# Kernel optimization log

Measured on AMD Instinct MI355X. Metric: run time of the kernel, lower is better.

Reference implementation:

```python
import jax, jax.numpy as jnp
import numpy as np

D_ATTN = 64


def setup_inputs() -> dict:
    key = jax.random.key(0)
    ks = jax.random.split(key, 10)
    B, N, D_MODEL = 8, 1024, 512
    s = 0.02
    return {
        "x": jax.random.normal(ks[0], (B, N, D_MODEL), jnp.float32),
        "top": jax.random.normal(ks[1], (B, N, N, 16), jnp.float32),
        "Wq": jax.random.normal(ks[2], (D_MODEL, D_ATTN), jnp.float32) * s,
        "bq": jnp.zeros((D_ATTN,), jnp.float32),
        "Wk": jax.random.normal(ks[3], (D_MODEL, D_ATTN), jnp.float32) * s,
        "bk": jnp.zeros((D_ATTN,), jnp.float32),
        "Wv": jax.random.normal(ks[4], (D_MODEL, D_ATTN), jnp.float32) * s,
        "bv": jnp.zeros((D_ATTN,), jnp.float32),
        "Wt": jax.random.normal(ks[5], (16, 1), jnp.float32) * s,
        "bt": jnp.zeros((1,), jnp.float32),
    }


def reference(x, top, Wq, bq, Wk, bk, Wv, bv, Wt, bt):
    # QKV projections: [B,N,d_model] -> [B,N,d_attn]
    Q = x @ Wq + bq
    K = x @ Wk + bk
    V = x @ Wv + bv
    scale = 1.0 / jnp.sqrt(jnp.asarray(D_ATTN, x.dtype))
    # [B,N,N] attention logits
    logits = jnp.einsum("bnd,bmd->bnm", Q, K) * scale
    # learned topological bias: Linear(16,1) on [B,N,N,16] -> [B,N,N]
    bias = jnp.einsum("bnmf,fo->bnmo", top, Wt)[..., 0] + bt[0]
    score = jax.nn.softmax(logits + bias, axis=-1)
    return jnp.einsum("bnm,bmd->bnd", score, V)
```

## Files before the change

kernel.cpp:

```cpp
#include <hip/hip_runtime.h>
#include <hip/hip_bf16.h>

typedef __attribute__((ext_vector_type(8))) short short8;
typedef __attribute__((ext_vector_type(4))) float f32x4;
typedef unsigned short ushort_t;
typedef unsigned int uint_t;

#define D_MODEL 512
#define D_ATTN  64

__device__ __forceinline__ ushort_t f2bf(float f) {
    uint_t u = __float_as_uint(f);
    u += 0x7FFFu + ((u >> 16) & 1u);
    return (ushort_t)(u >> 16);
}
__device__ __forceinline__ f32x4 ntload4(const f32x4* p) {
    return __builtin_nontemporal_load(p);
}

__global__ __launch_bounds__(256)
void qkv_all(const float* __restrict__ x,
             const float* __restrict__ Wq, const float* __restrict__ bq,
             const float* __restrict__ Wk, const float* __restrict__ bk,
             const float* __restrict__ Wv, const float* __restrict__ bv,
             ushort_t* __restrict__ Q, ushort_t* __restrict__ K,
             ushort_t* __restrict__ Vt)
{
    const int l = threadIdx.x & 63, w = threadIdx.x >> 6;
    const size_t bn0 = (size_t)blockIdx.x << 4;
    const int r0 = w << 2;
    const float* xb = x + (bn0 + r0) * D_MODEL;
    { uintptr_t u = (uintptr_t)xb; asm volatile("" : "+v"(u)); xb = (const float*)u; }

    float aq[4] = {0,0,0,0}, ak[4] = {0,0,0,0}, av[4] = {0,0,0,0};
#pragma unroll 2
    for (int k = 0; k < D_MODEL; k += 4) {
        float4 xr[4];
#pragma unroll
        for (int r = 0; r < 4; ++r) xr[r] = *(const float4*)(xb + r * D_MODEL + k);
        float wqv[4], wkv[4], wvv[4];
#pragma unroll
        for (int kk = 0; kk < 4; ++kk) {
            wqv[kk] = Wq[(k + kk) * D_ATTN + l];
            wkv[kk] = Wk[(k + kk) * D_ATTN + l];
            wvv[kk] = Wv[(k + kk) * D_ATTN + l];
        }
#pragma unroll
        for (int r = 0; r < 4; ++r) {
            const float xv[4] = {xr[r].x, xr[r].y, xr[r].z, xr[r].w};
#pragma unroll
            for (int kk = 0; kk < 4; ++kk) {
                aq[r] = fmaf(xv[kk], wqv[kk], aq[r]);
                ak[r] = fmaf(xv[kk], wkv[kk], ak[r]);
                av[r] = fmaf(xv[kk], wvv[kk], av[r]);
            }
        }
    }
    const float bqv = bq[l], bkv = bk[l], bvv = bv[l];
#pragma unroll
    for (int r = 0; r < 4; ++r) {
        Q[(bn0 + r0 + r) * D_ATTN + l] = f2bf((aq[r] + bqv) * 0.125f);
        K[(bn0 + r0 + r) * D_ATTN + l] = f2bf(ak[r] + bkv);
    }
    const int b = (int)(bn0 >> 10), n0loc = (int)(bn0 & 1023);
    uint2 pv;
    pv.x = (uint_t)f2bf(av[0] + bvv) | ((uint_t)f2bf(av[1] + bvv) << 16);
    pv.y = (uint_t)f2bf(av[2] + bvv) | ((uint_t)f2bf(av[3] + bvv) << 16);
    *(uint2*)(Vt + ((size_t)(b * 64 + l) << 10) + n0loc + r0) = pv;
}

__global__ __launch_bounds__(256)
void topo_attn_f(const float* __restrict__ top, const float* __restrict__ Wt,
                 const ushort_t* __restrict__ Q, const ushort_t* __restrict__ K,
                 const ushort_t* __restrict__ Vt, float* __restrict__ out)
{
    __shared__ float lds[16384];
    const int tid = threadIdx.x;
    const int l = tid & 63, wv = tid >> 6;
    const int b   = blockIdx.x >> 6;
    const int bn0 = blockIdx.x << 4;

    {
        const float* __restrict__ topb = top + ((size_t)bn0 << 14);
        const float4 wq = *(const float4*)(Wt + ((l & 3) << 2));
#pragma unroll
        for (int rr = 0; rr < 4; ++rr) {
            const int rloc = (wv << 2) + rr;
            const f32x4* gp = (const f32x4*)(topb + ((size_t)rloc << 14));
            float* ldsrow = lds + (rloc << 10);
#pragma unroll 2
            for (int g = 0; g < 16; ++g) {
                f32x4 v0 = ntload4(gp + (g << 8) + l);
                f32x4 v1 = ntload4(gp + (g << 8) + 64 + l);
                f32x4 v2 = ntload4(gp + (g << 8) + 128 + l);
                f32x4 v3 = ntload4(gp + (g << 8) + 192 + l);
                float p0 = v0[0] * wq.x; p0 = fmaf(v0[1], wq.y, p0); p0 = fmaf(v0[2], wq.z, p0); p0 = fmaf(v0[3], wq.w, p0);
                float p1 = v1[0] * wq.x; p1 = fmaf(v1[1], wq.y, p1); p1 = fmaf(v1[2], wq.z, p1); p1 = fmaf(v1[3], wq.w, p1);
                float p2 = v2[0] * wq.x; p2 = fmaf(v2[1], wq.y, p2); p2 = fmaf(v2[2], wq.z, p2); p2 = fmaf(v2[3], wq.w, p2);
                float p3 = v3[0] * wq.x; p3 = fmaf(v3[1], wq.y, p3); p3 = fmaf(v3[2], wq.z, p3); p3 = fmaf(v3[3], wq.w, p3);
                p0 += __shfl_xor(p0, 1); p0 += __shfl_xor(p0, 2);
                p1 += __shfl_xor(p1, 1); p1 += __shfl_xor(p1, 2);
                p2 += __shfl_xor(p2, 1); p2 += __shfl_xor(p2, 2);
                p3 += __shfl_xor(p3, 1); p3 += __shfl_xor(p3, 2);
                if (!(l & 3)) {
                    int mb = (g << 6) + (l >> 2);
                    ldsrow[mb]      = p0;
                    ldsrow[mb + 16] = p1;
                    ldsrow[mb + 32] = p2;
                    ldsrow[mb + 48] = p3;
                }
            }
        }
    }
    __syncthreads();

    const int lr = l & 15, lg = l >> 4;
    const short8 a0 = *(const short8*)(Q + ((size_t)(bn0 + lr)) * 64 + 8 * lg);
    const short8 a1 = *(const short8*)(Q + ((size_t)(bn0 + lr)) * 64 + 32 + 8 * lg);
    const ushort_t* __restrict__ Kb = K + ((size_t)b << 16);
#pragma unroll 4
    for (int t16 = 0; t16 < 16; ++t16) {
        int m0 = (wv << 8) + (t16 << 4);
        short8 kb0 = *(const short8*)(Kb + (size_t)(m0 + lr) * 64 + 8 * lg);
        short8 kb1 = *(const short8*)(Kb + (size_t)(m0 + lr) * 64 + 32 + 8 * lg);
        f32x4 acc = {0.f, 0.f, 0.f, 0.f};
        acc = __builtin_amdgcn_mfma_f32_16x16x32_bf16(a0, kb0, acc, 0, 0, 0);
        acc = __builtin_amdgcn_mfma_f32_16x16x32_bf16(a1, kb1, acc, 0, 0, 0);
#pragma unroll
        for (int j = 0; j < 4; ++j)
            lds[(4 * lg + j) * 1024 + m0 + lr] += acc[j];
    }
    __syncthreads();

    {
        const int r = tid >> 4, sseg = tid & 15;
        float4 v4[16];
        const float4* rowp = (const float4*)(lds + r * 1024 + sseg * 64);
#pragma unroll
        for (int i = 0; i < 16; ++i) v4[i] = rowp[i];
        __syncthreads();
        float mx = v4[0].x;
#pragma unroll
        for (int i = 0; i < 16; ++i)
            mx = fmaxf(mx, fmaxf(fmaxf(v4[i].x, v4[i].y), fmaxf(v4[i].z, v4[i].w)));
#pragma unroll
        for (int off = 8; off >= 1; off >>= 1) mx = fmaxf(mx, __shfl_xor(mx, off));
        float sum = 0.f;
#pragma unroll
        for (int i = 0; i < 16; ++i) {
            v4[i].x = __expf(v4[i].x - mx); sum += v4[i].x;
            v4[i].y = __expf(v4[i].y - mx); sum += v4[i].y;
            v4[i].z = __expf(v4[i].z - mx); sum += v4[i].z;
            v4[i].w = __expf(v4[i].w - mx); sum += v4[i].w;
        }
#pragma unroll
        for (int off = 8; off >= 1; off >>= 1) sum += __shfl_xor(sum, off);
        float inv = 1.0f / sum;
        ushort_t* pb = ((ushort_t*)lds) + r * 1024 + sseg * 64;
#pragma unroll
        for (int i = 0; i < 8; ++i) {
            uint_t w0 = (uint_t)f2bf(v4[2*i].x * inv)   | ((uint_t)f2bf(v4[2*i].y * inv)   << 16);
            uint_t w1 = (uint_t)f2bf(v4[2*i].z * inv)   | ((uint_t)f2bf(v4[2*i].w * inv)   << 16);
            uint_t w2 = (uint_t)f2bf(v4[2*i+1].x * inv) | ((uint_t)f2bf(v4[2*i+1].y * inv) << 16);
            uint_t w3 = (uint_t)f2bf(v4[2*i+1].z * inv) | ((uint_t)f2bf(v4[2*i+1].w * inv) << 16);
            ((uint4*)pb)[i] = make_uint4(w0, w1, w2, w3);
        }
    }
    __syncthreads();

    {
        f32x4 o[4] = {{0,0,0,0},{0,0,0,0},{0,0,0,0},{0,0,0,0}};
        const ushort_t* __restrict__ pb = ((const ushort_t*)lds) + lr * 1024;
        const ushort_t* __restrict__ Vb = Vt + ((size_t)b << 16);
#pragma unroll 2
        for (int c = 0; c < 8; ++c) {
            int m0 = (wv << 8) + (c << 5) + 8 * lg;
            short8 pa = *(const short8*)(pb + m0);
#pragma unroll
            for (int dt = 0; dt < 4; ++dt) {
                short8 vb = *(const short8*)(Vb + (size_t)(dt * 16 + lr) * 1024 + m0);
                o[dt] = __builtin_amdgcn_mfma_f32_16x16x32_bf16(pa, vb, o[dt], 0, 0, 0);
            }
        }
        float* lo = lds + 8192 + (wv << 10);
#pragma unroll
        for (int dt = 0; dt < 4; ++dt)
#pragma unroll
            for (int j = 0; j < 4; ++j)
                lo[(4 * lg + j) * 64 + dt * 16 + lr] = o[dt][j];
    }
    __syncthreads();

#pragma unroll
    for (int i = 0; i < 4; ++i) {
        int idx = (i << 8) + tid;
        float s2 = lds[8192 + idx] + lds[8192 + 1024 + idx]
                 + lds[8192 + 2048 + idx] + lds[8192 + 3072 + idx];
        out[((size_t)bn0 << 6) + idx] = s2;
    }
}

extern "C" void kernel_launch(void* const* d_in, const int* in_sizes, int n_in,
                              void* d_out, int out_size, void* d_ws, size_t ws_size,
                              hipStream_t stream) {
    const float* x   = (const float*)d_in[0];
    const float* top = (const float*)d_in[1];
    const float* Wq  = (const float*)d_in[2];
    const float* bq  = (const float*)d_in[3];
    const float* Wk  = (const float*)d_in[4];
    const float* bk  = (const float*)d_in[5];
    const float* Wv  = (const float*)d_in[6];
    const float* bv  = (const float*)d_in[7];
    const float* Wt  = (const float*)d_in[8];
    float* out = (float*)d_out;

    ushort_t* Q  = (ushort_t*)d_ws;
    ushort_t* K  = Q + 8 * 1024 * 64;
    ushort_t* Vt = K + 8 * 1024 * 64;

    qkv_all<<<512, 256, 0, stream>>>(x, Wq, bq, Wk, bk, Wv, bv, Q, K, Vt);
    topo_attn_f<<<512, 256, 0, stream>>>(top, Wt, Q, K, Vt, out);
}
```

Before: 164.5 us.

## Shrink LDS to bf16 bias tile, keep logits in registers, split PV by head dim

Stores the topological bias as bf16 in a padded shared tile, about 33KB instead of 64KB, and sets launch bounds to four blocks per CU to raise occupancy on this bandwidth-bound top stream. The top loads are software-pipelined one iteration ahead. QK^T logits stay in registers, and the softmax reduces across waves through small shared arrays. The PV product is split so each wave owns 16 output columns over all keys, which removes the cross-wave LDS reduction. The costs are bf16 rounding of the bias and extra register pressure from the 16 register-held logit tiles.

```diff
diff --git a/kernel.cpp b/kernel.cpp
--- a/kernel.cpp
+++ b/kernel.cpp
@@ -8,11 +8,15 @@
 
 #define D_MODEL 512
 #define D_ATTN  64
+#define LROW 1032
 
 __device__ __forceinline__ ushort_t f2bf(float f) {
     uint_t u = __float_as_uint(f);
     u += 0x7FFFu + ((u >> 16) & 1u);
     return (ushort_t)(u >> 16);
+}
+__device__ __forceinline__ float bf2f(ushort_t h) {
+    return __uint_as_float((uint_t)h << 16);
 }
 __device__ __forceinline__ f32x4 ntload4(const f32x4* p) {
     return __builtin_nontemporal_load(p);
@@ -69,134 +73,126 @@
     *(uint2*)(Vt + ((size_t)(b * 64 + l) << 10) + n0loc + r0) = pv;
 }
 
-__global__ __launch_bounds__(256)
+__global__ __launch_bounds__(256, 4)
 void topo_attn_f(const float* __restrict__ top, const float* __restrict__ Wt,
                  const ushort_t* __restrict__ Q, const ushort_t* __restrict__ K,
                  const ushort_t* __restrict__ Vt, float* __restrict__ out)
 {
-    __shared__ float lds[16384];
+    __shared__ ushort_t sm[16 * LROW];
+    __shared__ float redm[64], reds[64];
     const int tid = threadIdx.x;
     const int l = tid & 63, wv = tid >> 6;
     const int b   = blockIdx.x >> 6;
     const int bn0 = blockIdx.x << 4;
 
     {
-        const float* __restrict__ topb = top + ((size_t)bn0 << 14);
+        const f32x4* __restrict__ base = (const f32x4*)top + ((size_t)bn0 << 12);
         const float4 wq = *(const float4*)(Wt + ((l & 3) << 2));
-#pragma unroll
-        for (int rr = 0; rr < 4; ++rr) {
-            const int rloc = (wv << 2) + rr;
-            const f32x4* gp = (const f32x4*)(topb + ((size_t)rloc << 14));
-            float* ldsrow = lds + (rloc << 10);
-#pragma unroll 2
-            for (int g = 0; g < 16; ++g) {
-                f32x4 v0 = ntload4(gp + (g << 8) + l);
-                f32x4 v1 = ntload4(gp + (g << 8) + 64 + l);
-                f32x4 v2 = ntload4(gp + (g << 8) + 128 + l);
-                f32x4 v3 = ntload4(gp + (g << 8) + 192 + l);
-                float p0 = v0[0] * wq.x; p0 = fmaf(v0[1], wq.y, p0); p0 = fmaf(v0[2], wq.z, p0); p0 = fmaf(v0[3], wq.w, p0);
-                float p1 = v1[0] * wq.x; p1 = fmaf(v1[1], wq.y, p1); p1 = fmaf(v1[2], wq.z, p1); p1 = fmaf(v1[3], wq.w, p1);
-                float p2 = v2[0] * wq.x; p2 = fmaf(v2[1], wq.y, p2); p2 = fmaf(v2[2], wq.z, p2); p2 = fmaf(v2[3], wq.w, p2);
-                float p3 = v3[0] * wq.x; p3 = fmaf(v3[1], wq.y, p3); p3 = fmaf(v3[2], wq.z, p3); p3 = fmaf(v3[3], wq.w, p3);
-                p0 += __shfl_xor(p0, 1); p0 += __shfl_xor(p0, 2);
-                p1 += __shfl_xor(p1, 1); p1 += __shfl_xor(p1, 2);
-                p2 += __shfl_xor(p2, 1); p2 += __shfl_xor(p2, 2);
-                p3 += __shfl_xor(p3, 1); p3 += __shfl_xor(p3, 2);
-                if (!(l & 3)) {
-                    int mb = (g << 6) + (l >> 2);
-                    ldsrow[mb]      = p0;
-                    ldsrow[mb + 16] = p1;
-                    ldsrow[mb + 32] = p2;
-                    ldsrow[mb + 48] = p3;
-                }
+        const int sel = l & 3;
+        const f32x4* p0a = base + ((size_t)(wv << 2) << 12) + l;
+        f32x4 c0 = ntload4(p0a), c1 = ntload4(p0a + 64),
+              c2 = ntload4(p0a + 128), c3 = ntload4(p0a + 192);
+        for (int it = 0; it < 64; ++it) {
+            f32x4 n0, n1, n2, n3;
+            if (it < 63) {
+                int it1 = it + 1;
+                const f32x4* q = base + ((size_t)((wv << 2) + (it1 >> 4)) << 12)
+                                      + ((it1 & 15) << 8) + l;
+                n0 = ntload4(q); n1 = ntload4(q + 64);
+                n2 = ntload4(q + 128); n3 = ntload4(q + 192);
             }
+            float p0 = c0[0] * wq.x; p0 = fmaf(c0[1], wq.y, p0); p0 = fmaf(c0[2], wq.z, p0); p0 = fmaf(c0[3], wq.w, p0);
+            float p1 = c1[0] * wq.x; p1 = fmaf(c1[1], wq.y, p1); p1 = fmaf(c1[2], wq.z, p1); p1 = fmaf(c1[3], wq.w, p1);
+            float p2 = c2[0] * wq.x; p2 = fmaf(c2[1], wq.y, p2); p2 = fmaf(c2[2], wq.z, p2); p2 = fmaf(c2[3], wq.w, p2);
+            float p3 = c3[0] * wq.x; p3 = fmaf(c3[1], wq.y, p3); p3 = fmaf(c3[2], wq.z, p3); p3 = fmaf(c3[3], wq.w, p3);
+            p0 += __shfl_xor(p0, 1); p0 += __shfl_xor(p0, 2);
+            p1 += __shfl_xor(p1, 1); p1 += __shfl_xor(p1, 2);
+            p2 += __shfl_xor(p2, 1); p2 += __shfl_xor(p2, 2);
+            p3 += __shfl_xor(p3, 1); p3 += __shfl_xor(p3, 2);
+            float pr = (sel == 0) ? p0 : (sel == 1) ? p1 : (sel == 2) ? p2 : p3;
+            int rloc = (wv << 2) + (it >> 4);
+            int m = ((it & 15) << 6) + (l >> 2) + (sel << 4);
+            sm[rloc * LROW + m] = f2bf(pr);
+            c0 = n0; c1 = n1; c2 = n2; c3 = n3;
         }
     }
     __syncthreads();
 
-    const int lr = l & 15, lg = l >> 4;
-    const short8 a0 = *(const short8*)(Q + ((size_t)(bn0 + lr)) * 64 + 8 * lg);
-    const short8 a1 = *(const short8*)(Q + ((size_t)(bn0 + lr)) * 64 + 32 + 8 * lg);
-    const ushort_t* __restrict__ Kb = K + ((size_t)b << 16);
+    const int lq = l & 15, lg4 = l >> 4;
+    f32x4 lgt[16];
+    {
+        const short8 qb0 = *(const short8*)(Q + ((size_t)(bn0 + lq)) * 64 + 8 * lg4);
+        const short8 qb1 = *(const short8*)(Q + ((size_t)(bn0 + lq)) * 64 + 32 + 8 * lg4);
+        const ushort_t* __restrict__ Kb = K + ((size_t)b << 16);
 #pragma unroll 4
-    for (int t16 = 0; t16 < 16; ++t16) {
-        int m0 = (wv << 8) + (t16 << 4);
-        short8 kb0 = *(const short8*)(Kb + (size_t)(m0 + lr) * 64 + 8 * lg);
-        short8 kb1 = *(const short8*)(Kb + (size_t)(m0 + lr) * 64 + 32 + 8 * lg);
-        f32x4 acc = {0.f, 0.f, 0.f, 0.f};
-        acc = __builtin_amdgcn_mfma_f32_16x16x32_bf16(a0, kb0, acc, 0, 0, 0);
-        acc = __builtin_amdgcn_mfma_f32_16x16x32_bf16(a1, kb1, acc, 0, 0, 0);
+        for (int t = 0; t < 16; ++t) {
+            int m0 = (wv << 8) + (t << 4);
+            short8 kb0 = *(const short8*)(Kb + (size_t)(m0 + lq) * 64 + 8 * lg4);
+            short8 kb1 = *(const short8*)(Kb + (size_t)(m0 + lq) * 64 + 32 + 8 * lg4);
+            f32x4 acc = {0.f, 0.f, 0.f, 0.f};
+            acc = __builtin_amdgcn_mfma_f32_16x16x32_bf16(kb0, qb0, acc, 0, 0, 0);
+            acc = __builtin_amdgcn_mfma_f32_16x16x32_bf16(kb1, qb1, acc, 0, 0, 0);
+#pragma unroll
+            for (int j = 0; j < 4; ++j)
+                acc[j] += bf2f(sm[lq * LROW + m0 + 4 * lg4 + j]);
+            lgt[t] = acc;
+        }
+    }
+
+    {
+        float mx = lgt[0][0];
+#pragma unroll
+        for (int t = 0; t < 16; ++t)
+#pragma unroll
+            for (int j = 0; j < 4; ++j) mx = fmaxf(mx, lgt[t][j]);
+        mx = fmaxf(mx, __shfl_xor(mx, 16));
+        mx = fmaxf(mx, __shfl_xor(mx, 32));
+        if (l < 16) redm[l * 4 + wv] = mx;
+        __syncthreads();
+        float gmx = fmaxf(fmaxf(redm[lq * 4 + 0], redm[lq * 4 + 1]),
+                          fmaxf(redm[lq * 4 + 2], redm[lq * 4 + 3]));
+        float s = 0.f;
+#pragma unroll
+        for (int t = 0; t < 16; ++t)
+#pragma unroll
+            for (int j = 0; j < 4; ++j) {
+                float e = __expf(lgt[t][j] - gmx);
+                lgt[t][j] = e; s += e;
+            }
+        s += __shfl_xor(s, 16);
+        s += __shfl_xor(s, 32);
+        if (l < 16) reds[l * 4 + wv] = s;
+        __syncthreads();
+        float inv = 1.0f / (reds[lq * 4 + 0] + reds[lq * 4 + 1]
+                          + reds[lq * 4 + 2] + reds[lq * 4 + 3]);
+#pragma unroll
+        for (int t = 0; t < 16; ++t) {
+            int mbase = (wv << 8) + (t << 4) + 4 * lg4;
+            uint_t w01 = (uint_t)f2bf(lgt[t][0] * inv) | ((uint_t)f2bf(lgt[t][1] * inv) << 16);
+            uint_t w23 = (uint_t)f2bf(lgt[t][2] * inv) | ((uint_t)f2bf(lgt[t][3] * inv) << 16);
+            *(uint_t*)(sm + lq * LROW + mbase)     = w01;
+            *(uint_t*)(sm + lq * LROW + mbase + 2) = w23;
+        }
+    }
+    __syncthreads();
+
+    {
+        f32x4 oe = {0,0,0,0}, oo = {0,0,0,0};
+        const ushort_t* __restrict__ Vb = Vt + ((size_t)b << 16)
+                                        + ((size_t)((wv << 4) + lq) << 10);
+        const ushort_t* __restrict__ pb = sm + lq * LROW + 8 * lg4;
+#pragma unroll 4
+        for (int kk = 0; kk < 32; kk += 2) {
+            short8 pa0 = *(const short8*)(pb + (kk << 5));
+            short8 vb0 = *(const short8*)(Vb + (kk << 5) + 8 * lg4);
+            oe = __builtin_amdgcn_mfma_f32_16x16x32_bf16(pa0, vb0, oe, 0, 0, 0);
+            short8 pa1 = *(const short8*)(pb + (kk << 5) + 32);
+            short8 vb1 = *(const short8*)(Vb + (kk << 5) + 32 + 8 * lg4);
+            oo = __builtin_amdgcn_mfma_f32_16x16x32_bf16(pa1, vb1, oo, 0, 0, 0);
+        }
 #pragma unroll
         for (int j = 0; j < 4; ++j)
-            lds[(4 * lg + j) * 1024 + m0 + lr] += acc[j];
-    }
-    __syncthreads();
-
-    {
-        const int r = tid >> 4, sseg = tid & 15;
-        float4 v4[16];
-        const float4* rowp = (const float4*)(lds + r * 1024 + sseg * 64);
-#pragma unroll
-        for (int i = 0; i < 16; ++i) v4[i] = rowp[i];
-        __syncthreads();
-        float mx = v4[0].x;
-#pragma unroll
-        for (int i = 0; i < 16; ++i)
-            mx = fmaxf(mx, fmaxf(fmaxf(v4[i].x, v4[i].y), fmaxf(v4[i].z, v4[i].w)));
-#pragma unroll
-        for (int off = 8; off >= 1; off >>= 1) mx = fmaxf(mx, __shfl_xor(mx, off));
-        float sum = 0.f;
-#pragma unroll
-        for (int i = 0; i < 16; ++i) {
-            v4[i].x = __expf(v4[i].x - mx); sum += v4[i].x;
-            v4[i].y = __expf(v4[i].y - mx); sum += v4[i].y;
-            v4[i].z = __expf(v4[i].z - mx); sum += v4[i].z;
-            v4[i].w = __expf(v4[i].w - mx); sum += v4[i].w;
-        }
-#pragma unroll
-        for (int off = 8; off >= 1; off >>= 1) sum += __shfl_xor(sum, off);
-        float inv = 1.0f / sum;
-        ushort_t* pb = ((ushort_t*)lds) + r * 1024 + sseg * 64;
-#pragma unroll
-        for (int i = 0; i < 8; ++i) {
-            uint_t w0 = (uint_t)f2bf(v4[2*i].x * inv)   | ((uint_t)f2bf(v4[2*i].y * inv)   << 16);
-            uint_t w1 = (uint_t)f2bf(v4[2*i].z * inv)   | ((uint_t)f2bf(v4[2*i].w * inv)   << 16);
-            uint_t w2 = (uint_t)f2bf(v4[2*i+1].x * inv) | ((uint_t)f2bf(v4[2*i+1].y * inv) << 16);
-            uint_t w3 = (uint_t)f2bf(v4[2*i+1].z * inv) | ((uint_t)f2bf(v4[2*i+1].w * inv) << 16);
-            ((uint4*)pb)[i] = make_uint4(w0, w1, w2, w3);
-        }
-    }
-    __syncthreads();
-
-    {
-        f32x4 o[4] = {{0,0,0,0},{0,0,0,0},{0,0,0,0},{0,0,0,0}};
-        const ushort_t* __restrict__ pb = ((const ushort_t*)lds) + lr * 1024;
-        const ushort_t* __restrict__ Vb = Vt + ((size_t)b << 16);
-#pragma unroll 2
-        for (int c = 0; c < 8; ++c) {
-            int m0 = (wv << 8) + (c << 5) + 8 * lg;
-            short8 pa = *(const short8*)(pb + m0);
-#pragma unroll
-            for (int dt = 0; dt < 4; ++dt) {
-                short8 vb = *(const short8*)(Vb + (size_t)(dt * 16 + lr) * 1024 + m0);
-                o[dt] = __builtin_amdgcn_mfma_f32_16x16x32_bf16(pa, vb, o[dt], 0, 0, 0);
-            }
-        }
-        float* lo = lds + 8192 + (wv << 10);
-#pragma unroll
-        for (int dt = 0; dt < 4; ++dt)
-#pragma unroll
-            for (int j = 0; j < 4; ++j)
-                lo[(4 * lg + j) * 64 + dt * 16 + lr] = o[dt][j];
-    }
-    __syncthreads();
-
-#pragma unroll
-    for (int i = 0; i < 4; ++i) {
-        int idx = (i << 8) + tid;
-        float s2 = lds[8192 + idx] + lds[8192 + 1024 + idx]
-                 + lds[8192 + 2048 + idx] + lds[8192 + 3072 + idx];
-        out[((size_t)bn0 << 6) + idx] = s2;
+            out[((size_t)(bn0 + 4 * lg4 + j) << 6) + (wv << 4) + lq] = oe[j] + oo[j];
     }
 }
 
```

After: 179.0 us. +8.9%, slower.
